# Kernel tuning notes

Hardware: AMD Instinct MI355X
Metric: run time of the kernel (lower is better)

The kernel has to match this reference:

```python
import jax, jax.numpy as jnp
import numpy as np
from jax import lax

IMG_SIZE = 1024
NUM_CLASSES = 80
TOP_K = 300          # self.top_k
CLS_THRES = 0.05     # self.cls_thres
IOU_THR = 0.5        # nms overlap
BBOX_STD = jnp.array([0.1, 0.1, 0.2, 0.2], dtype=jnp.float32)


def make_anchors(img_size=IMG_SIZE):
    """Standard RetinaNet anchors: P3-P7, 3 ratios x 3 scales per cell."""
    strides = [8, 16, 32, 64, 128]
    ratios = np.array([0.5, 1.0, 2.0])
    scales = 2.0 ** (np.arange(3) / 3.0)
    out = []
    for s in strides:
        base = 4.0 * s
        ws, hs = [], []
        for r in ratios:
            for sc in scales:
                ws.append(base * sc / np.sqrt(r))
                hs.append(base * sc * np.sqrt(r))
        ws = np.array(ws); hs = np.array(hs)  # [9]
        fs = img_size // s
        shift = (np.arange(fs) + 0.5) * s
        cy, cx = np.meshgrid(shift, shift, indexing='ij')
        cx = cx.ravel()[:, None]; cy = cy.ravel()[:, None]
        a = np.stack([cx - ws / 2, cy - hs / 2, cx + ws / 2, cy + hs / 2], axis=-1)
        out.append(a.reshape(-1, 4))
    return np.concatenate(out, axis=0).astype(np.float32)  # [A,4]


def setup_inputs() -> dict:
    key = jax.random.key(0)
    k1, k2 = jax.random.split(key)
    anchors = jnp.asarray(make_anchors())[None]          # [1,A,4]
    A = anchors.shape[1]
    classifications = jax.random.uniform(k1, (1, A, NUM_CLASSES), dtype=jnp.float32)
    regressions = jax.random.normal(k2, (1, A, 4), dtype=jnp.float32)
    return {"classifications": classifications, "regressions": regressions,
            "anchors": anchors, "img_h": IMG_SIZE, "img_w": IMG_SIZE}


def decode_boxes(anchors, regressions):
    # BBoxTransform: mean=0, std=[.1,.1,.2,.2]
    w = anchors[..., 2] - anchors[..., 0]
    h = anchors[..., 3] - anchors[..., 1]
    cx = anchors[..., 0] + 0.5 * w
    cy = anchors[..., 1] + 0.5 * h
    d = regressions * BBOX_STD
    pcx = cx + d[..., 0] * w
    pcy = cy + d[..., 1] * h
    pw = jnp.exp(d[..., 2]) * w
    ph = jnp.exp(d[..., 3]) * h
    return jnp.stack([pcx - 0.5 * pw, pcy - 0.5 * ph,
                      pcx + 0.5 * pw, pcy + 0.5 * ph], axis=-1)


def pairwise_iou(b):  # b: [K,4]
    x1, y1, x2, y2 = b[:, 0], b[:, 1], b[:, 2], b[:, 3]
    area = jnp.clip(x2 - x1, 0) * jnp.clip(y2 - y1, 0)
    iw = jnp.clip(jnp.minimum(x2[:, None], x2[None]) - jnp.maximum(x1[:, None], x1[None]), 0)
    ih = jnp.clip(jnp.minimum(y2[:, None], y2[None]) - jnp.maximum(y1[:, None], y1[None]), 0)
    inter = iw * ih
    return inter / (area[:, None] + area[None] - inter + 1e-8)


def nms_one_class(boxes, scores_c):
    """Greedy NMS over top-K candidates above threshold for one class."""
    s = jnp.where(scores_c > CLS_THRES, scores_c, -jnp.inf)
    top_scores, top_idx = lax.top_k(s, TOP_K)        # sorted descending
    cand_valid = top_scores > CLS_THRES
    iou = pairwise_iou(boxes[top_idx])               # [K,K]
    idxs = jnp.arange(TOP_K)

    def body(suppressed, i):
        sup_i = suppressed[i] | (~cand_valid[i])
        new_sup = suppressed | ((~sup_i) & (iou[i] > IOU_THR) & (idxs > i))
        return new_sup, ~sup_i

    _, keep = lax.scan(body, jnp.zeros(TOP_K, bool), idxs)
    return top_idx, top_scores, keep


def reference(classifications, regressions, anchors, img_h, img_w):
    boxes = decode_boxes(anchors, regressions)       # [1,A,4]
    boxes = jnp.stack([jnp.maximum(boxes[..., 0], 0.0),
                       jnp.maximum(boxes[..., 1], 0.0),
                       jnp.minimum(boxes[..., 2], float(img_w)),
                       jnp.minimum(boxes[..., 3], float(img_h))], axis=-1)
    boxes0 = boxes[0]                                # [A,4]  (batch item 0, as original)
    cls0 = classifications[0]                        # [A,C]
    A, C = cls0.shape

    # per-class NMS, vmapped over the class axis
    top_idx, top_scores, keep = jax.vmap(nms_one_class, in_axes=(None, 1))(boxes0, cls0)
    # scatter kept scores back into dense [A,C] matrix (original 'scores' tensor)
    scores_mat = jnp.zeros((A, C), cls0.dtype).at[top_idx, jnp.arange(C)[:, None]].set(
        jnp.where(keep, top_scores, 0.0))

    scores_max = scores_mat.max(axis=1)
    labels = scores_mat.argmax(axis=1)
    valid = scores_max > 0
    # fixed-shape (jit-friendly) equivalent of the original's boolean filtering:
    final_scores = jnp.where(valid, scores_max, 0.0)
    final_labels = jnp.where(valid, labels, -1)
    final_boxes = jnp.where(valid[:, None], boxes0, 0.0)
    return final_scores, final_labels, final_boxes
```

## Files before the change

### kernel.cpp

```cpp
#include <hip/hip_runtime.h>
#include <cstdint>

typedef unsigned long long u64;
typedef unsigned int u32;

#define CLS_T    0.05f
#define T1G      0.9965f
#define TOPK     300
#define NWORDS   5
#define HBINS    2560
#define KEY_BASE 0x3D000000u
#define CCAP     1024
#define NBLK     2048
#define SCAP     16
#define OVBIT    0x80000000u

__device__ inline u32 bin_of_bits(u32 bits) {
    u32 b = (bits - KEY_BASE) >> 14;
    if (b > (HBINS - 1)) b = HBINS - 1;
    return b;
}

__device__ inline float4 decode_box(const float* __restrict__ anc,
                                    const float* __restrict__ reg,
                                    u32 a, float W, float H)
{
    float x1 = anc[(size_t)a*4+0], y1 = anc[(size_t)a*4+1];
    float x2 = anc[(size_t)a*4+2], y2 = anc[(size_t)a*4+3];
    float w = x2 - x1, h = y2 - y1;
    float cx = x1 + 0.5f*w, cy = y1 + 0.5f*h;
    float r0 = reg[(size_t)a*4+0]*0.1f, r1 = reg[(size_t)a*4+1]*0.1f;
    float r2 = reg[(size_t)a*4+2]*0.2f, r3 = reg[(size_t)a*4+3]*0.2f;
    float pcx = cx + r0*w, pcy = cy + r1*h;
    float pw_ = expf(r2)*w, ph_ = expf(r3)*h;
    float4 b;
    b.x = fmaxf(pcx - 0.5f*pw_, 0.0f);
    b.y = fmaxf(pcy - 0.5f*ph_, 0.0f);
    b.z = fminf(pcx + 0.5f*pw_, W);
    b.w = fminf(pcy + 0.5f*ph_, H);
    return b;
}

__device__ inline void cex(u64& v, u64 p, bool lo, bool up) {
    u64 mx = v > p ? v : p;
    u64 mn = v > p ? p : v;
    v = (lo == up) ? mx : mn;
}
__device__ inline void sstep(u64& a0, u64& a1, u32 tid, u32 kk, u32 j) {
    u64 p0 = __shfl_xor((unsigned long long)a0, (int)j, 64);
    u64 p1 = __shfl_xor((unsigned long long)a1, (int)j, 64);
    bool lo = ((tid & j) == 0);
    cex(a0, p0, lo, ((tid & kk) == 0));
    cex(a1, p1, lo, (((tid + 512u) & kk) == 0));
}
__device__ inline void lstep640(u64* cand, u64& a0, u64& a1, u32 tid, u32 kk, u32 j) {
    __syncthreads();
    if (tid < 512) { cand[tid] = a0; cand[tid + 512] = a1; }
    __syncthreads();
    if (tid < 512) {
        u64 p0 = cand[tid ^ j], p1 = cand[(tid ^ j) + 512];
        bool lo = ((tid & j) == 0);
        cex(a0, p0, lo, ((tid & kk) == 0));
        cex(a1, p1, lo, (((tid + 512u) & kk) == 0));
    }
}

__global__ void decode_kernel(const float* __restrict__ anc,
                              const float* __restrict__ reg,
                              const int* __restrict__ ph,
                              const int* __restrict__ pw,
                              float* __restrict__ boxes,
                              u64* __restrict__ akey, int A)
{
    int a = blockIdx.x * blockDim.x + threadIdx.x;
    if (a >= A) return;
    akey[a] = 0;
    float W = (float)(*pw), H = (float)(*ph);
    float4 b = decode_box(anc, reg, (u32)a, W, H);
    boxes[a*4+0] = b.x; boxes[a*4+1] = b.y;
    boxes[a*4+2] = b.z; boxes[a*4+3] = b.w;
}

__global__ __launch_bounds__(256) void fused_scan_kernel(
    const float* __restrict__ cls,
    u64* __restrict__ akey,
    u64* __restrict__ gbuf, u32* __restrict__ segcnt, int A)
{
    const int tid = threadIdx.x;
    const int blk = blockIdx.x;

    for (int a = blk * 256 + tid; a < A; a += NBLK * 256) akey[a] = 0;

    __shared__ u32 cnt[80];
    __shared__ u64 buf[80][SCAP];
    __shared__ u32 s_over;
    for (int i = tid; i < 80; i += 256) cnt[i] = 0;
    if (tid == 0) s_over = 0;
    __syncthreads();

    size_t Nf4 = (size_t)A * 20;
    const float4* p4 = (const float4*)cls;
    for (size_t i = (size_t)blk * 256 + tid; i < Nf4; i += (size_t)NBLK * 256) {
        float4 v = p4[i];
        float ss[4] = {v.x, v.y, v.z, v.w};
        #pragma unroll
        for (int q = 0; q < 4; ++q) {
            if (ss[q] > T1G) {
                u32 flat = (u32)(i * 4 + q);
                u32 a = flat / 80u;
                u32 c = flat - a * 80u;
                u32 p = atomicAdd(&cnt[c], 1u);
                if (p < SCAP) buf[c][p] = ((u64)__float_as_uint(ss[q]) << 32) | (u32)(~a);
                else s_over = 1;
            }
        }
    }
    __syncthreads();

    const u32 ob = s_over ? OVBIT : 0u;
    for (int m = tid; m < 80 * SCAP; m += 256) {
        int c = m / SCAP, e = m - c * SCAP;
        u32 cc = cnt[c]; if (cc > SCAP) cc = SCAP;
        if ((u32)e < cc)
            gbuf[((size_t)c * NBLK + blk) * SCAP + e] = buf[c][e];
    }
    for (int c = tid; c < 80; c += 256) {
        u32 cc = cnt[c]; if (cc > SCAP) cc = SCAP;
        segcnt[(size_t)c * NBLK + blk] = cc | ob;
    }
}

__global__ __launch_bounds__(640) void class_fused_kernel(
    const u32* __restrict__ segcnt, const u64* __restrict__ gbuf,
    const float* __restrict__ cls,
    const float* __restrict__ anc, const float* __restrict__ reg,
    const int* __restrict__ ph, const int* __restrict__ pw,
    u64* __restrict__ akey, int A, int C)
{
    const int c = blockIdx.x;
    const u32 tid = threadIdx.x;
    const int lane = tid & 63;

    __shared__ u32 sh[HBINS];
    __shared__ u32 sp[NBLK];
    __shared__ u64 cand[CCAP];
    __shared__ u32 s_sel, s_cnt, s_rem, s_ob;
    __shared__ float4 sbox[TOPK];
    __shared__ float  sbar[TOPK];
    __shared__ u64 iomaskT[NWORDS][TOPK];
    __shared__ u64 s_keep[NWORDS];

    if (tid == 0) { s_sel = 0; s_cnt = 0; s_ob = 0; }
    __syncthreads();

    const float W = (float)(*pw), H = (float)(*ph);

    u32 v[4] = {0,0,0,0};
    u32 s = 0;
    if (tid < 512) {
        const u32* row = segcnt + (size_t)c * NBLK;
        u32 ob = 0;
        #pragma unroll
        for (int q = 0; q < 4; ++q) {
            u32 r = row[tid * 4 + q];
            ob |= r & OVBIT;
            v[q] = r & ~OVBIT;
            s += v[q];
        }
        if (ob) atomicOr(&s_ob, 1u);
        sh[tid] = s;
    }
    __syncthreads();
    for (int d = 1; d < 512; d <<= 1) {
        u32 t2 = (tid >= (u32)d && tid < 512) ? sh[tid - d] : 0;
        __syncthreads();
        if (tid < 512) sh[tid] += t2;
        __syncthreads();
    }
    if (tid < 512) {
        u32 run = sh[tid] - s;
        #pragma unroll
        for (int q = 0; q < 4; ++q) { sp[tid * 4 + q] = run; run += v[q]; }
    }
    __syncthreads();
    const u32 n = sh[511];
    const bool over = (s_ob != 0);
    __syncthreads();

    u32 cnt_f = 0;
    bool fast_ok = false;

    if (!over && n >= TOPK && n <= CCAP) {
        for (u32 i = tid; i < n; i += 640) {
            int lo = 0, hi = NBLK;
            while (hi - lo > 1) {
                int mid = (lo + hi) >> 1;
                if (sp[mid] <= i) lo = mid; else hi = mid;
            }
            u32 e = i - sp[lo];
            cand[i] = gbuf[((size_t)c * NBLK + lo) * SCAP + e];
        }
        __syncthreads();
        cnt_f = n;
        fast_ok = true;
    }

    if (!fast_ok) {
        __syncthreads();
        for (int i = tid; i < HBINS; i += 640) sh[i] = 0;
        if (tid == 0) s_cnt = 0;
        __syncthreads();
        for (int a = tid; a < A; a += 640) {
            float sc = cls[(size_t)a * C + c];
            if (sc > CLS_T) atomicAdd(&sh[bin_of_bits(__float_as_uint(sc))], 1u);
        }
        __syncthreads();
        if (tid == 0) {
            u32 cum = 0; int sel = 0;
            for (int d = HBINS - 1; d >= 0; --d) {
                u32 nc = cum + sh[d];
                if (nc >= TOPK) { sel = d; break; }
                cum = nc;
            }
            s_sel = (u32)sel; s_rem = TOPK - cum;
        }
        __syncthreads();
        const u32 sel1 = s_sel;
        __syncthreads();
        for (int i = tid; i < 256; i += 640) sh[i] = 0;
        __syncthreads();
        for (int a = tid; a < A; a += 640) {
            float sc = cls[(size_t)a * C + c];
            if (sc > CLS_T) {
                u32 k = __float_as_uint(sc) - KEY_BASE;
                u32 b = k >> 14; if (b >= HBINS) b = HBINS - 1;
                if (b == sel1) atomicAdd(&sh[(k >> 6) & 0xFF], 1u);
            }
        }
        __syncthreads();
        if (tid == 0) {
            u32 rem = s_rem, cum = 0; int sel = 0;
            for (int d = 255; d >= 0; --d) {
                u32 nc = cum + sh[d];
                if (nc >= rem) { sel = d; break; }
                cum = nc;
            }
            s_sel = (sel1 << 14) | ((u32)sel << 6);
            s_cnt = 0;
        }
        __syncthreads();
        const u32 thresh = s_sel;
        for (int a = tid; a < A; a += 640) {
            float sc = cls[(size_t)a * C + c];
            if (sc > CLS_T) {
                u32 bits = __float_as_uint(sc);
                if (bits - KEY_BASE >= thresh) {
                    u32 p = atomicAdd(&s_cnt, 1u);
                    if (p < CCAP) cand[p] = ((u64)bits << 32) | (u32)(~(u32)a);
                }
            }
        }
        __syncthreads();
        cnt_f = s_cnt < CCAP ? s_cnt : CCAP;
    }

    for (u32 i = cnt_f + tid; i < CCAP; i += 640) cand[i] = 0;
    for (int m = tid; m < NWORDS * TOPK; m += 640) ((u64*)iomaskT)[m] = 0;
    __syncthreads();

    u64 a0 = 0, a1 = 0;
    if (tid < 512) { a0 = cand[tid]; a1 = cand[tid + 512]; }
    if (tid < 512)
        for (u32 kk = 2; kk <= 64; kk <<= 1)
            for (u32 j = kk >> 1; j >= 1; j >>= 1)
                sstep(a0, a1, tid, kk, j);
    lstep640(cand, a0, a1, tid, 128u, 64u);
    if (tid < 512) for (u32 j = 32; j >= 1; j >>= 1) sstep(a0, a1, tid, 128u, j);
    lstep640(cand, a0, a1, tid, 256u, 128u);
    lstep640(cand, a0, a1, tid, 256u, 64u);
    if (tid < 512) for (u32 j = 32; j >= 1; j >>= 1) sstep(a0, a1, tid, 256u, j);
    lstep640(cand, a0, a1, tid, 512u, 256u);
    lstep640(cand, a0, a1, tid, 512u, 128u);
    lstep640(cand, a0, a1, tid, 512u, 64u);
    if (tid < 512) for (u32 j = 32; j >= 1; j >>= 1) sstep(a0, a1, tid, 512u, j);
    if (tid < 512) {
        u64 mx = a0 > a1 ? a0 : a1, mn = a0 > a1 ? a1 : a0;
        a0 = mx; a1 = mn;
    }
    lstep640(cand, a0, a1, tid, 1024u, 256u);
    lstep640(cand, a0, a1, tid, 1024u, 128u);
    lstep640(cand, a0, a1, tid, 1024u, 64u);
    if (tid < 512) for (u32 j = 32; j >= 1; j >>= 1) sstep(a0, a1, tid, 1024u, j);

    const int T = (int)(cnt_f < TOPK ? cnt_f : TOPK);

    u64 key = a0; u32 aidx = 0;
    if ((int)tid < T) {
        aidx = ~(u32)(key & 0xFFFFFFFFull);
        float4 b4 = decode_box(anc, reg, aidx, W, H);
        sbox[tid] = b4;
        sbar[tid] = fmaxf(b4.z - b4.x, 0.0f) * fmaxf(b4.w - b4.y, 0.0f);
    }
    __syncthreads();

    {
        const int jj = (int)(tid < 320 ? tid : tid - 320);
        const int p  = (int)(tid < 320 ? 0 : 1);
        if (jj < T) {
            float4 b = sbox[jj];
            float ar = sbar[jj];
            u64 cm[NWORDS] = {0,0,0,0,0};
            for (int i = p; i < jj; i += 2) {
                float4 bi = sbox[i];
                float iw = fmaxf(fminf(b.z, bi.z) - fmaxf(b.x, bi.x), 0.0f);
                float ih = fmaxf(fminf(b.w, bi.w) - fmaxf(b.y, bi.y), 0.0f);
                float inter = iw * ih;
                float uni = ((ar + sbar[i]) - inter) + 1e-8f;
                if (inter / uni > 0.5f) cm[i >> 6] |= 1ull << (i & 63);
            }
            #pragma unroll
            for (int w = 0; w < NWORDS; ++w)
                if (cm[w]) atomicOr(&iomaskT[w][jj], cm[w]);
        }
    }
    __syncthreads();

    if (tid < 64) {
        u64 K[NWORDS];
        #pragma unroll
        for (int w = 0; w < NWORDS; ++w) {
            int b = w * 64 + lane;
            bool valid = (b < T);
            u64 cmw = 0, se = 0;
            if (valid) {
                #pragma unroll
                for (int w2 = 0; w2 < NWORDS; ++w2)
                    if (w2 < w) se |= K[w2] & iomaskT[w2][b];
                cmw = iomaskT[w][b];
            }
            u64 U = __ballot(valid && se == 0);
            u64 Kw = 0;
            int guard = 0;
            while (U && guard++ < 64) {
                u64 newk = __ballot(((U >> lane) & 1ull) && ((cmw & U) == 0));
                Kw |= newk; U &= ~newk;
                u64 supp = __ballot((cmw & Kw) != 0);
                U &= ~supp;
            }
            K[w] = Kw;
        }
        if (lane == 0) {
            #pragma unroll
            for (int w = 0; w < NWORDS; ++w) s_keep[w] = K[w];
        }
    }
    __syncthreads();

    if ((int)tid < T) {
        if ((s_keep[tid >> 6] >> (tid & 63)) & 1ull) {
            u32 sbits = (u32)(key >> 32);
            u64 outk = ((u64)sbits << 32) | (u32)(255 - c);
            atomicMax(&akey[aidx], outk);
        }
    }
}

__global__ void finalize_kernel(const u64* __restrict__ akey,
                                const float* __restrict__ anc,
                                const float* __restrict__ reg,
                                const int* __restrict__ ph,
                                const int* __restrict__ pw,
                                float* __restrict__ out, int A)
{
    int a = blockIdx.x * blockDim.x + threadIdx.x;
    if (a >= A) return;
    float* scores = out;
    float* labels = out + A;
    float* boxes  = out + (size_t)2 * A;
    u64 k = akey[a];
    if (k) {
        scores[a] = __uint_as_float((u32)(k >> 32));
        labels[a] = (float)(int)(255u - (u32)(k & 0xFFFFFFFFull));
        float W = (float)(*pw), H = (float)(*ph);
        float4 b = decode_box(anc, reg, (u32)a, W, H);
        boxes[(size_t)a*4+0] = b.x; boxes[(size_t)a*4+1] = b.y;
        boxes[(size_t)a*4+2] = b.z; boxes[(size_t)a*4+3] = b.w;
    } else {
        scores[a] = 0.0f;
        labels[a] = -1.0f;
        boxes[(size_t)a*4+0] = 0.0f;
        boxes[(size_t)a*4+1] = 0.0f;
        boxes[(size_t)a*4+2] = 0.0f;
        boxes[(size_t)a*4+3] = 0.0f;
    }
}

__global__ void fb_finalize_kernel(const u64* __restrict__ akey,
                                   float* __restrict__ out, int A)
{
    int a = blockIdx.x * blockDim.x + threadIdx.x;
    if (a >= A) return;
    float* scores = out;
    float* labels = out + A;
    float* boxes  = out + (size_t)2 * A;
    u64 k = akey[a];
    if (k) {
        scores[a] = __uint_as_float((u32)(k >> 32));
        labels[a] = (float)(int)(255u - (u32)(k & 0xFFFFFFFFull));
    } else {
        scores[a] = 0.0f;
        labels[a] = -1.0f;
        boxes[(size_t)a*4+0] = 0.0f;
        boxes[(size_t)a*4+1] = 0.0f;
        boxes[(size_t)a*4+2] = 0.0f;
        boxes[(size_t)a*4+3] = 0.0f;
    }
}

#define FB_CAP 1024
__global__ __launch_bounds__(256) void fb_topk_nms_kernel(
    const float* __restrict__ cls,
    const float* __restrict__ boxes,
    u64* __restrict__ akey,
    int A, int C)
{
    const int c   = blockIdx.x;
    const int tid = threadIdx.x;

    __shared__ u32 hist[HBINS];
    __shared__ u64 cand[FB_CAP];
    __shared__ float bx1[TOPK], by1[TOPK], bx2[TOPK], by2[TOPK], bar[TOPK];
    __shared__ u64 iomask[TOPK][NWORDS];
    __shared__ u64 keepm[NWORDS];
    __shared__ u32 s_sel1, s_sel2, s_rem, s_cnt;

    for (int i = tid; i < HBINS; i += 256) hist[i] = 0;
    __syncthreads();
    for (int a = tid; a < A; a += 256) {
        float s = cls[(size_t)a * C + c];
        if (s > CLS_T) {
            u32 k = __float_as_uint(s) - KEY_BASE;
            u32 b = k >> 14; if (b >= HBINS) b = HBINS - 1;
            atomicAdd(&hist[b], 1u);
        }
    }
    __syncthreads();
    if (tid == 0) {
        u32 cum = 0; int sel = 0;
        for (int d = HBINS - 1; d >= 0; --d) {
            u32 nc = cum + hist[d];
            if (nc >= TOPK) { sel = d; break; }
            cum = nc;
        }
        s_sel1 = (u32)sel; s_rem = TOPK - cum;
    }
    __syncthreads();
    const u32 sel1 = s_sel1;

    for (int i = tid; i < 256; i += 256) hist[i] = 0;
    __syncthreads();
    for (int a = tid; a < A; a += 256) {
        float s = cls[(size_t)a * C + c];
        if (s > CLS_T) {
            u32 k = __float_as_uint(s) - KEY_BASE;
            u32 b = k >> 14; if (b >= HBINS) b = HBINS - 1;
            if (b == sel1) atomicAdd(&hist[(k >> 6) & 0xFF], 1u);
        }
    }
    __syncthreads();
    if (tid == 0) {
        u32 rem = s_rem, cum = 0; int sel = 0;
        for (int d = 255; d >= 0; --d) {
            u32 nc = cum + hist[d];
            if (nc >= rem) { sel = d; break; }
            cum = nc;
        }
        s_sel2 = (u32)sel; s_cnt = 0;
    }
    __syncthreads();
    const u32 thresh = (sel1 << 14) | (s_sel2 << 6);

    for (int a = tid; a < A; a += 256) {
        float s = cls[(size_t)a * C + c];
        if (s > CLS_T) {
            u32 bits = __float_as_uint(s);
            u32 k = bits - KEY_BASE;
            if (k >= thresh) {
                u32 pos = atomicAdd(&s_cnt, 1u);
                if (pos < FB_CAP) cand[pos] = ((u64)bits << 32) | (u32)(~(u32)a);
            }
        }
    }
    __syncthreads();
    const u32 total = s_cnt < FB_CAP ? s_cnt : FB_CAP;
    for (int i = tid; i < FB_CAP; i += 256)
        if (i >= (int)total) cand[i] = 0;
    __syncthreads();

    for (u32 kk = 2; kk <= FB_CAP; kk <<= 1) {
        for (u32 j = kk >> 1; j > 0; j >>= 1) {
            for (u32 i = tid; i < FB_CAP; i += 256) {
                u32 l = i ^ j;
                if (l > i) {
                    u64 av = cand[i], bv = cand[l];
                    bool up = ((i & kk) == 0);
                    if ((up && av < bv) || (!up && av > bv)) { cand[i] = bv; cand[l] = av; }
                }
            }
            __syncthreads();
        }
    }
    const int T = (int)(total < TOPK ? total : TOPK);

    for (int i = tid; i < T; i += 256) {
        u32 a = ~(u32)(cand[i] & 0xFFFFFFFFull);
        float x1 = boxes[(size_t)a*4+0], y1 = boxes[(size_t)a*4+1];
        float x2 = boxes[(size_t)a*4+2], y2 = boxes[(size_t)a*4+3];
        bx1[i] = x1; by1[i] = y1; bx2[i] = x2; by2[i] = y2;
        bar[i] = fmaxf(x2 - x1, 0.0f) * fmaxf(y2 - y1, 0.0f);
    }
    __syncthreads();

    for (int i = tid; i < T; i += 256) {
        u64 m[NWORDS] = {0,0,0,0,0};
        float x1 = bx1[i], y1 = by1[i], x2 = bx2[i], y2 = by2[i], ai = bar[i];
        for (int j = i + 1; j < T; ++j) {
            float iw = fmaxf(fminf(x2, bx2[j]) - fmaxf(x1, bx1[j]), 0.0f);
            float ih = fmaxf(fminf(y2, by2[j]) - fmaxf(y1, by1[j]), 0.0f);
            float inter = iw * ih;
            float uni = ((ai + bar[j]) - inter) + 1e-8f;
            if (inter / uni > 0.5f) m[j >> 6] |= 1ull << (j & 63);
        }
        for (int k2 = 0; k2 < NWORDS; ++k2) iomask[i][k2] = m[k2];
    }
    __syncthreads();

    if (tid == 0) {
        u64 sup[NWORDS] = {0,0,0,0,0};
        u64 kp [NWORDS] = {0,0,0,0,0};
        for (int i = 0; i < T; ++i) {
            if (!((sup[i >> 6] >> (i & 63)) & 1ull)) {
                kp[i >> 6] |= 1ull << (i & 63);
                for (int k2 = 0; k2 < NWORDS; ++k2) sup[k2] |= iomask[i][k2];
            }
        }
        for (int k2 = 0; k2 < NWORDS; ++k2) keepm[k2] = kp[k2];
    }
    __syncthreads();

    for (int i = tid; i < T; i += 256) {
        if ((keepm[i >> 6] >> (i & 63)) & 1ull) {
            u64 key = cand[i];
            u32 a = ~(u32)(key & 0xFFFFFFFFull);
            u32 sbits = (u32)(key >> 32);
            u64 outk = ((u64)sbits << 32) | (u32)(255 - c);
            atomicMax(&akey[a], outk);
        }
    }
}

extern "C" void kernel_launch(void* const* d_in, const int* in_sizes, int n_in,
                              void* d_out, int out_size, void* d_ws, size_t ws_size,
                              hipStream_t stream) {
    const float* cls = (const float*)d_in[0];
    const float* reg = (const float*)d_in[1];
    const float* anc = (const float*)d_in[2];
    const int*   ph  = (const int*)d_in[3];
    const int*   pw  = (const int*)d_in[4];

    int A = in_sizes[2] / 4;
    int C = in_sizes[0] / A;

    float* out       = (float*)d_out;
    float* out_boxes = out + (size_t)2 * A;

    size_t akey_bytes = (size_t)A * sizeof(u64);
    size_t off_sc     = (akey_bytes + 255) & ~(size_t)255;
    size_t sc_bytes   = (size_t)80 * NBLK * sizeof(u32);
    size_t off_gb     = (off_sc + sc_bytes + 255) & ~(size_t)255;
    size_t gb_bytes   = (size_t)80 * NBLK * SCAP * sizeof(u64);
    size_t need       = off_gb + gb_bytes;

    u64* akey = (u64*)d_ws;

    bool fastpath = (C == 80) && ((A & 3) == 0) && (A < (1 << 20)) && (ws_size >= need);

    if (fastpath) {
        u32* segcnt = (u32*)((char*)d_ws + off_sc);
        u64* gbuf   = (u64*)((char*)d_ws + off_gb);

        fused_scan_kernel<<<NBLK, 256, 0, stream>>>(cls, akey, gbuf, segcnt, A);
        class_fused_kernel<<<C, 640, 0, stream>>>(segcnt, gbuf, cls, anc, reg, ph, pw, akey, A, C);
        finalize_kernel<<<(A + 255) / 256, 256, 0, stream>>>(akey, anc, reg, ph, pw, out, A);
    } else {
        decode_kernel<<<(A + 255) / 256, 256, 0, stream>>>(anc, reg, ph, pw, out_boxes, akey, A);
        fb_topk_nms_kernel<<<C, 256, 0, stream>>>(cls, out_boxes, akey, A, C);
        fb_finalize_kernel<<<(A + 255) / 256, 256, 0, stream>>>(akey, out, A);
    }
}
```

Before: 57.27 us.

## Halve candidate capacity to 512 and replace block scan with wave-shuffle scan

Raises the global pre-filter threshold so fewer candidates per class are expected, halves the candidate buffer to 512, and simplifies the bitonic sort to one element per thread, which drops the final 1024-wide merge stages. It also replaces the barrier-heavy shared-memory prefix scan of segment counts with a wave-level shuffle scan plus a small cross-wave reduction, and drops a redundant barrier. The threshold is tuned to the uniform test distribution, so more classes may overflow into the slow histogram fallback path when counts exceed 512.

After: 51.82 us. 1.11x faster.

```diff
diff --git a/kernel.cpp b/kernel.cpp
--- a/kernel.cpp
+++ b/kernel.cpp
@@ -5,12 +5,12 @@
 typedef unsigned int u32;
 
 #define CLS_T    0.05f
-#define T1G      0.9965f
+#define T1G      0.997933f
 #define TOPK     300
 #define NWORDS   5
 #define HBINS    2560
 #define KEY_BASE 0x3D000000u
-#define CCAP     1024
+#define CCAP     512
 #define NBLK     2048
 #define SCAP     16
 #define OVBIT    0x80000000u
@@ -46,22 +46,17 @@
     u64 mn = v > p ? p : v;
     v = (lo == up) ? mx : mn;
 }
-__device__ inline void sstep(u64& a0, u64& a1, u32 tid, u32 kk, u32 j) {
-    u64 p0 = __shfl_xor((unsigned long long)a0, (int)j, 64);
-    u64 p1 = __shfl_xor((unsigned long long)a1, (int)j, 64);
-    bool lo = ((tid & j) == 0);
-    cex(a0, p0, lo, ((tid & kk) == 0));
-    cex(a1, p1, lo, (((tid + 512u) & kk) == 0));
-}
-__device__ inline void lstep640(u64* cand, u64& a0, u64& a1, u32 tid, u32 kk, u32 j) {
-    __syncthreads();
-    if (tid < 512) { cand[tid] = a0; cand[tid + 512] = a1; }
+__device__ inline void s1(u64& v, u32 tid, u32 kk, u32 j) {
+    u64 p = __shfl_xor((unsigned long long)v, (int)j, 64);
+    cex(v, p, (tid & j) == 0, (tid & kk) == 0);
+}
+__device__ inline void l1(u64* sm, u64& v, u32 tid, u32 kk, u32 j) {
+    __syncthreads();
+    if (tid < 512) sm[tid] = v;
     __syncthreads();
     if (tid < 512) {
-        u64 p0 = cand[tid ^ j], p1 = cand[(tid ^ j) + 512];
-        bool lo = ((tid & j) == 0);
-        cex(a0, p0, lo, ((tid & kk) == 0));
-        cex(a1, p1, lo, (((tid + 512u) & kk) == 0));
+        u64 p = sm[tid ^ j];
+        cex(v, p, (tid & j) == 0, (tid & kk) == 0);
     }
 }
 
@@ -144,48 +139,55 @@
     __shared__ u32 sh[HBINS];
     __shared__ u32 sp[NBLK];
     __shared__ u64 cand[CCAP];
-    __shared__ u32 s_sel, s_cnt, s_rem, s_ob;
+    __shared__ u32 wtot[8], wob[8];
+    __shared__ u32 s_sel, s_cnt, s_rem;
     __shared__ float4 sbox[TOPK];
     __shared__ float  sbar[TOPK];
     __shared__ u64 iomaskT[NWORDS][TOPK];
     __shared__ u64 s_keep[NWORDS];
 
-    if (tid == 0) { s_sel = 0; s_cnt = 0; s_ob = 0; }
-    __syncthreads();
-
     const float W = (float)(*pw), H = (float)(*ph);
 
-    u32 v[4] = {0,0,0,0};
-    u32 s = 0;
+    u32 v4[4] = {0,0,0,0};
+    u32 s = 0, ob = 0;
     if (tid < 512) {
         const u32* row = segcnt + (size_t)c * NBLK;
-        u32 ob = 0;
         #pragma unroll
         for (int q = 0; q < 4; ++q) {
             u32 r = row[tid * 4 + q];
             ob |= r & OVBIT;
-            v[q] = r & ~OVBIT;
-            s += v[q];
-        }
-        if (ob) atomicOr(&s_ob, 1u);
-        sh[tid] = s;
-    }
-    __syncthreads();
-    for (int d = 1; d < 512; d <<= 1) {
-        u32 t2 = (tid >= (u32)d && tid < 512) ? sh[tid - d] : 0;
-        __syncthreads();
-        if (tid < 512) sh[tid] += t2;
-        __syncthreads();
+            v4[q] = r & ~OVBIT;
+            s += v4[q];
+        }
+    }
+    u32 incl = s;
+    #pragma unroll
+    for (int d = 1; d < 64; d <<= 1) {
+        u32 t = __shfl_up(incl, d, 64);
+        if ((tid & 63) >= (u32)d) incl += t;
+    }
+    u64 obm = __ballot(ob != 0);
+    if (tid < 512 && (tid & 63) == 63) {
+        wtot[tid >> 6] = incl;
+        wob [tid >> 6] = (obm != 0) ? 1u : 0u;
+    }
+    __syncthreads();
+    u32 woff = 0, ntot = 0, obt = 0;
+    #pragma unroll
+    for (int w2 = 0; w2 < 8; ++w2) {
+        u32 t = wtot[w2];
+        obt |= wob[w2];
+        if (w2 < (int)(tid >> 6)) woff += t;
+        ntot += t;
     }
     if (tid < 512) {
-        u32 run = sh[tid] - s;
+        u32 base = woff + incl - s;
         #pragma unroll
-        for (int q = 0; q < 4; ++q) { sp[tid * 4 + q] = run; run += v[q]; }
-    }
-    __syncthreads();
-    const u32 n = sh[511];
-    const bool over = (s_ob != 0);
-    __syncthreads();
+        for (int q = 0; q < 4; ++q) { sp[tid * 4 + q] = base; base += v4[q]; }
+    }
+    __syncthreads();
+    const u32 n = ntot;
+    const bool over = (obt != 0);
 
     u32 cnt_f = 0;
     bool fast_ok = false;
@@ -200,7 +202,6 @@
             u32 e = i - sp[lo];
             cand[i] = gbuf[((size_t)c * NBLK + lo) * SCAP + e];
         }
-        __syncthreads();
         cnt_f = n;
         fast_ok = true;
     }
@@ -268,33 +269,26 @@
     for (int m = tid; m < NWORDS * TOPK; m += 640) ((u64*)iomaskT)[m] = 0;
     __syncthreads();
 
-    u64 a0 = 0, a1 = 0;
-    if (tid < 512) { a0 = cand[tid]; a1 = cand[tid + 512]; }
-    if (tid < 512)
+    u64 v = 0;
+    if (tid < 512) {
+        v = cand[tid];
         for (u32 kk = 2; kk <= 64; kk <<= 1)
             for (u32 j = kk >> 1; j >= 1; j >>= 1)
-                sstep(a0, a1, tid, kk, j);
-    lstep640(cand, a0, a1, tid, 128u, 64u);
-    if (tid < 512) for (u32 j = 32; j >= 1; j >>= 1) sstep(a0, a1, tid, 128u, j);
-    lstep640(cand, a0, a1, tid, 256u, 128u);
-    lstep640(cand, a0, a1, tid, 256u, 64u);
-    if (tid < 512) for (u32 j = 32; j >= 1; j >>= 1) sstep(a0, a1, tid, 256u, j);
-    lstep640(cand, a0, a1, tid, 512u, 256u);
-    lstep640(cand, a0, a1, tid, 512u, 128u);
-    lstep640(cand, a0, a1, tid, 512u, 64u);
-    if (tid < 512) for (u32 j = 32; j >= 1; j >>= 1) sstep(a0, a1, tid, 512u, j);
-    if (tid < 512) {
-        u64 mx = a0 > a1 ? a0 : a1, mn = a0 > a1 ? a1 : a0;
-        a0 = mx; a1 = mn;
-    }
-    lstep640(cand, a0, a1, tid, 1024u, 256u);
-    lstep640(cand, a0, a1, tid, 1024u, 128u);
-    lstep640(cand, a0, a1, tid, 1024u, 64u);
-    if (tid < 512) for (u32 j = 32; j >= 1; j >>= 1) sstep(a0, a1, tid, 1024u, j);
+                s1(v, tid, kk, j);
+    }
+    l1(cand, v, tid, 128u, 64u);
+    if (tid < 512) for (u32 j = 32; j >= 1; j >>= 1) s1(v, tid, 128u, j);
+    l1(cand, v, tid, 256u, 128u);
+    l1(cand, v, tid, 256u, 64u);
+    if (tid < 512) for (u32 j = 32; j >= 1; j >>= 1) s1(v, tid, 256u, j);
+    l1(cand, v, tid, 512u, 256u);
+    l1(cand, v, tid, 512u, 128u);
+    l1(cand, v, tid, 512u, 64u);
+    if (tid < 512) for (u32 j = 32; j >= 1; j >>= 1) s1(v, tid, 512u, j);
 
     const int T = (int)(cnt_f < TOPK ? cnt_f : TOPK);
 
-    u64 key = a0; u32 aidx = 0;
+    u64 key = v; u32 aidx = 0;
     if ((int)tid < T) {
         aidx = ~(u32)(key & 0xFFFFFFFFull);
         float4 b4 = decode_box(anc, reg, aidx, W, H);
```
